# Optimization experiments

Measured on AMD Instinct MI355X. Metric: run time of the kernel, lower is better.

The kernel has to match this reference:

```python
import jax, jax.numpy as jnp
import numpy as np

T, B, L, S = 2048, 64, 32, 256
NEG = -1e30  # effective -inf, safe under logaddexp


def setup_inputs() -> dict:
    key = jax.random.key(0)
    k1, k2, k3 = jax.random.split(key, 3)
    inputs = jax.random.normal(k1, (T, B, L), dtype=jnp.float32)
    targets = jax.random.randint(k2, (B, S), 0, L)
    input_lengths = jnp.full((B,), T, dtype=jnp.int32)
    target_lengths = jnp.full((B,), S, dtype=jnp.int32)
    # learned transition matrix (param of ASGLoss); small random for a non-trivial test
    transition = 0.1 * jax.random.normal(k3, (L, L), dtype=jnp.float32)
    return {"transition": transition, "inputs": inputs, "targets": targets,
            "input_lengths": input_lengths, "target_lengths": target_lengths}


def _fcc_scores(transition, inputs, input_lengths):
    # Fully-connected forward: alpha_t[i] = emit_t[i] + logsumexp_j(alpha_{t-1}[j] + trans[i,j])
    alpha0 = inputs[0]  # [B, L]

    def step(alpha, emit):
        new = emit + jax.nn.logsumexp(alpha[:, None, :] + transition[None, :, :], axis=2)
        return new, new

    _, rest = jax.lax.scan(step, alpha0, inputs[1:])
    alphas = jnp.concatenate([alpha0[None], rest], axis=0)  # [T, B, L]
    b = jnp.arange(inputs.shape[1])
    # causal DP: alpha at t = len-1 is exactly the score for that length
    return jax.nn.logsumexp(alphas[input_lengths - 1, b], axis=-1)  # [B]


def _fac_scores(transition, inputs, targets, input_lengths, target_lengths):
    # Force-aligned forward over target positions s:
    # alpha_t[s] = emit_t[tgt_s] + logaddexp(alpha_{t-1}[s] + trans[tgt_s,tgt_s],
    #                                        alpha_{t-1}[s-1] + trans[tgt_s,tgt_{s-1}])
    Tn, Bn, _ = inputs.shape
    Sn = targets.shape[1]
    # gathered emissions for target labels: [T, B, S]
    emit = jnp.take_along_axis(inputs, jnp.broadcast_to(targets[None], (Tn, Bn, Sn)), axis=2)
    self_tr = transition[targets, targets]                       # [B, S] stay score
    prev = jnp.concatenate([targets[:, :1], targets[:, :-1]], 1)
    move_tr = transition[targets, prev]                          # [B, S] move score (s=0 unused)

    alpha0 = jnp.where((jnp.arange(Sn) == 0)[None, :], emit[0], NEG)  # only s=0 at t=0

    def step(alpha, e):
        stay = alpha + self_tr
        moved = jnp.concatenate(
            [jnp.full_like(alpha[:, :1], NEG), alpha[:, :-1] + move_tr[:, 1:]], axis=1)
        new = e + jnp.logaddexp(stay, moved)
        return new, new

    _, rest = jax.lax.scan(step, alpha0, emit[1:])
    alphas = jnp.concatenate([alpha0[None], rest], axis=0)  # [T, B, S]
    b = jnp.arange(Bn)
    return alphas[input_lengths - 1, b, target_lengths - 1]  # [B]


def reference(transition, inputs, targets, input_lengths, target_lengths):
    # original clamps targets to input length; S <= T here so it's a no-op
    fcc = _fcc_scores(transition, inputs, input_lengths)
    fac = _fac_scores(transition, inputs, targets, input_lengths, target_lengths)
    result = fcc - fac  # [B]
    return result.mean()  # reduction='mean'
```

## Files before the change

### kernel.cpp

```cpp
#include <hip/hip_runtime.h>
#include <math.h>

static constexpr int TB = 64;
static constexpr int LL = 32;
static constexpr int SS = 256;
static constexpr int STRIDE_T = TB * LL;

static constexpr int OF_FWD  = 0;
static constexpr int OF_BWD  = 33;
static constexpr int OF_FACF = 2178;
static constexpr int OF_FACB = 2498;
static constexpr int WSB     = 2818;

#define LN2F 0.69314718055994530942f
#define NEGF (-1e30f)

#define BARX() { asm volatile("s_waitcnt lgkmcnt(0)" ::: "memory"); \
                 __builtin_amdgcn_s_barrier(); \
                 asm volatile("" ::: "memory"); }

template<int CTL>
__device__ __forceinline__ float dpp_f(float x, float oldv) {
  return __int_as_float(__builtin_amdgcn_update_dpp(
      __float_as_int(oldv), __float_as_int(x), CTL, 0xF, 0xF, false));
}
template<int M>
__device__ __forceinline__ int rot_i(int x) {
  return __builtin_amdgcn_update_dpp(0, x, 0x120 + M, 0xF, 0xF, false);
}

typedef unsigned uint2v __attribute__((ext_vector_type(2)));
__device__ __forceinline__ float xsum16(float x) {
  uint2v r = __builtin_amdgcn_permlane16_swap(__float_as_uint(x), __float_as_uint(x), false, false);
  return __uint_as_float(r.x) + __uint_as_float(r.y);
}
__device__ __forceinline__ float xsum32(float x) {
  uint2v r = __builtin_amdgcn_permlane32_swap(__float_as_uint(x), __float_as_uint(x), false, false);
  return __uint_as_float(r.x) + __uint_as_float(r.y);
}
__device__ __forceinline__ float bperm(int addr, float src) {
  return __int_as_float(__builtin_amdgcn_ds_bpermute(addr, __float_as_int(src)));
}

template<int M>
struct Calib {
  __device__ static __forceinline__ void run(const float* trans, int lam, int i, float* Ec) {
    Ec[M] = __expf(trans[i * LL + rot_i<M>(lam)]);
    Calib<M + 1>::run(trans, lam, i, Ec);
  }
};
template<> struct Calib<16> {
  __device__ static __forceinline__ void run(const float*, int, int, float*) {}
};
template<int M>
struct CalibT {
  __device__ static __forceinline__ void run(const float* trans, int lam, int i, float* Ec) {
    Ec[M] = __expf(trans[rot_i<M>(lam) * LL + i]);
    CalibT<M + 1>::run(trans, lam, i, Ec);
  }
};
template<> struct CalibT<16> {
  __device__ static __forceinline__ void run(const float*, int, int, float*) {}
};

#define ROT_MUL(DST, SRC, COEF, ROT) \
  asm("v_mul_f32_dpp %0, %1, %2 row_ror:" #ROT " row_mask:0xf bank_mask:0xf" \
      : "=v"(DST) : "v"(SRC), "v"(COEF))
#define ROT_FMAC(ACC, SRC, COEF, ROT) \
  asm("v_fmac_f32_dpp %0, %1, %2 row_ror:" #ROT " row_mask:0xf bank_mask:0xf" \
      : "+v"(ACC) : "v"(SRC), "v"(COEF))

#define STEP16(EC) { \
  float a0 = EC[0] * A, a1, a2, a3, a4, a5, a6, a7; \
  ROT_MUL(a1, A, EC[1], 1); ROT_MUL(a2, A, EC[2], 2); ROT_MUL(a3, A, EC[3], 3); \
  ROT_MUL(a4, A, EC[4], 4); ROT_MUL(a5, A, EC[5], 5); ROT_MUL(a6, A, EC[6], 6); \
  ROT_MUL(a7, A, EC[7], 7); \
  ROT_FMAC(a0, A, EC[8], 8);   ROT_FMAC(a1, A, EC[9], 9); \
  ROT_FMAC(a2, A, EC[10], 10); ROT_FMAC(a3, A, EC[11], 11); \
  ROT_FMAC(a4, A, EC[12], 12); ROT_FMAC(a5, A, EC[13], 13); \
  ROT_FMAC(a6, A, EC[14], 14); ROT_FMAC(a7, A, EC[15], 15); \
  part = ((a0 + a1) + (a2 + a3)) + ((a4 + a5) + (a6 + a7)); }


#define FCC_RENORM() { \
  unsigned uu = (unsigned)__builtin_amdgcn_readfirstlane((int)__float_as_uint(A)); \
  int ex = (int)((uu >> 23) & 255) - 127; \
  A = ldexpf(A, -ex); Kt += ex; }

#define FCC_STEP_E(Q) { float part; STEP16(Ec1); A = eb[Q] * xsum16(part); }
#define FCC_STEP_O(Q) { float part; STEP16(Ec2); A = eb[Q] * xsum32(part); }

#define FCC_CONSUME16(PB) { \
  float eb[16]; \
  _Pragma("unroll") for (int q = 0; q < 16; ++q) eb[q] = sE[PB][q][(q & 1) ? lam1 : lam2]; \
  FCC_STEP_E(0); FCC_STEP_O(1); FCC_STEP_E(2); FCC_STEP_O(3); \
  FCC_STEP_E(4); FCC_STEP_O(5); FCC_STEP_E(6); FCC_STEP_O(7); \
  FCC_RENORM(); \
  FCC_STEP_E(8); FCC_STEP_O(9); FCC_STEP_E(10); FCC_STEP_O(11); \
  FCC_STEP_E(12); FCC_STEP_O(13); FCC_STEP_E(14); FCC_STEP_O(15); \
  FCC_RENORM(); }

#define FCC_TAIL16(PB, CNT) { \
  float eb[16]; \
  _Pragma("unroll") for (int q = 0; q < 16; ++q) eb[q] = sE[PB][q][(q & 1) ? lam1 : lam2]; \
  _Pragma("unroll") for (int q = 0; q < 16; ++q) { \
    if (q >= (CNT)) break; \
    if ((q & 1) == 0) { float part; STEP16(Ec1); A = eb[q] * xsum16(part); } \
    else              { float part; STEP16(Ec2); A = eb[q] * xsum32(part); } \
    if (q == 7) { FCC_RENORM(); } } }

#define FCC_BSTEP_A(Q) { A *= eb[Q]; float part; STEP16(E1T); A = xsum16(part); }
#define FCC_BSTEP_B(Q) { A *= eb[Q]; float part; STEP16(E2T); A = xsum32(part); }

#define FCC_BWDCON16(PB) { \
  float eb[16]; \
  _Pragma("unroll") for (int q = 0; q < 16; ++q) eb[q] = sE[PB][q][(q & 1) ? lam1 : lam2]; \
  FCC_BSTEP_A(15); FCC_BSTEP_B(14); FCC_BSTEP_A(13); FCC_BSTEP_B(12); \
  FCC_BSTEP_A(11); FCC_BSTEP_B(10); FCC_BSTEP_A(9);  FCC_BSTEP_B(8); \
  FCC_RENORM(); \
  FCC_BSTEP_A(7);  FCC_BSTEP_B(6);  FCC_BSTEP_A(5);  FCC_BSTEP_B(4); \
  FCC_BSTEP_A(3);  FCC_BSTEP_B(2);  FCC_BSTEP_A(1);  FCC_BSTEP_B(0); \
  FCC_RENORM(); }


#define FAC_STEP(E0, E1, E2, E3) { \
  float ap = dpp_f<0x138>(A3, 0.f);  \
  float n0 = (E0) * fmaf(MV0b,  ap, ST[0] * A0); \
  float n1 = (E1) * fmaf(MVl[1], A0, ST[1] * A1); \
  float n2 = (E2) * fmaf(MVl[2], A1, ST[2] * A2); \
  float n3 = (E3) * fmaf(MVl[3], A2, ST[3] * A3); \
  A0 = n0; A1 = n1; A2 = n2; A3 = n3; }

#define FAC_BOUNDARY() { \
  float maxA = fmaxf(fmaxf(A0, A1), fmaxf(A2, A3)); \
  if (maxA > 0.f) { \
    int ex = (int)((__float_as_uint(maxA) >> 23) & 255) - 127; \
    A0 = ldexpf(A0, -ex); A1 = ldexpf(A1, -ex); \
    A2 = ldexpf(A2, -ex); A3 = ldexpf(A3, -ex); \
    m += (float)ex; \
  } \
  float mp = dpp_f<0x138>(m, NEGF); m = (m == NEGF) ? mp : m; \
  mp = dpp_f<0x138>(m, NEGF);       m = (m == NEGF) ? mp : m; \
  mp = dpp_f<0x138>(m, NEGF); \
  float dlt = fminf(mp - m, 50.0f); \
  float Sin = exp2f(dlt); \
  MV0b = MVl[0] * Sin; }

#define FACF_CON16(PB) { \
  float4 Er[16]; \
  _Pragma("unroll") for (int r = 0; r < 16; ++r) Er[r] = sF[PB][r][l]; \
  _Pragma("unroll") for (int r = 0; r < 8; ++r) \
    FAC_STEP(Er[r].x, Er[r].y, Er[r].z, Er[r].w); \
  FAC_BOUNDARY(); \
  _Pragma("unroll") for (int r = 8; r < 16; ++r) \
    FAC_STEP(Er[r].x, Er[r].y, Er[r].z, Er[r].w); \
  FAC_BOUNDARY(); }

#define FACF_TAIL16(PB, CNT) { \
  float4 Er[16]; \
  _Pragma("unroll") for (int r = 0; r < 16; ++r) Er[r] = sF[PB][r][l]; \
  _Pragma("unroll") for (int r = 0; r < 16; ++r) { \
    if (r >= (CNT)) break; \
    FAC_STEP(Er[r].x, Er[r].y, Er[r].z, Er[r].w); \
    if (r == 7) { FAC_BOUNDARY(); } } }

#define FACB_BOUNDARY() { \
  float maxA = fmaxf(fmaxf(A0, A1), fmaxf(A2, A3)); \
  if (maxA > 0.f) { \
    int ex = (int)((__float_as_uint(maxA) >> 23) & 255) - 127; \
    A0 = ldexpf(A0, -ex); A1 = ldexpf(A1, -ex); \
    A2 = ldexpf(A2, -ex); A3 = ldexpf(A3, -ex); \
    m += (float)ex; \
  } \
  float mp = dpp_f<0x130>(m, NEGF); m = (m == NEGF) ? mp : m; \
  mp = dpp_f<0x130>(m, NEGF);       m = (m == NEGF) ? mp : m; \
  mp = dpp_f<0x130>(m, NEGF); \
  float dlt = fminf(mp - m, 50.0f); \
  MVn3b = MVn[3] * exp2f(dlt); }

#define FACB_STEP(Q) { \
    float en3 = dpp_f<0x130>(Er[Q].x, 0.f);  \
    float an  = dpp_f<0x130>(A0, 0.f); \
    float n0 = fmaf(Er[Q].y * MVn[0], A1, Er[Q].x * ST[0] * A0); \
    float n1 = fmaf(Er[Q].z * MVn[1], A2, Er[Q].y * ST[1] * A1); \
    float n2 = fmaf(Er[Q].w * MVn[2], A3, Er[Q].z * ST[2] * A2); \
    float n3 = fmaf(en3 * MVn3b,      an, Er[Q].w * ST[3] * A3); \
    A0 = n0; A1 = n1; A2 = n2; A3 = n3; }

#define FACB_CON16(PB) { \
  float4 Er[16]; \
  _Pragma("unroll") for (int r = 0; r < 16; ++r) Er[r] = sF[PB][r][l]; \
  FACB_STEP(15); FACB_STEP(14); FACB_STEP(13); FACB_STEP(12); \
  FACB_STEP(11); FACB_STEP(10); FACB_STEP(9);  FACB_STEP(8); \
  FACB_BOUNDARY(); \
  FACB_STEP(7);  FACB_STEP(6);  FACB_STEP(5);  FACB_STEP(4); \
  FACB_STEP(3);  FACB_STEP(2);  FACB_STEP(1);  FACB_STEP(0); \
  FACB_BOUNDARY(); }


#define HLD(Q, K) ({ \
  int tt_ = (isfwd ? (1 + 16 * (Q)) : (lenm1 - 16 * (Q) - 15)) + 2 * (K) + rowoff; \
  tt_ = tt_ < 0 ? 0 : (tt_ > lenm1 ? lenm1 : tt_); \
  gpl[(size_t)tt_ * STRIDE_T]; })

#define PROD_FCC(PB, KK, RV) { sE[PB][2 * (KK) + rowoff][lam1] = __expf(RV); }

#define PROD_FAC(PB, KK, RV) { \
  float e_ = __expf(RV); \
  float4 E0_, E1_; \
  E0_.x = bperm(adA[0], e_); E0_.y = bperm(adA[1], e_); \
  E0_.z = bperm(adA[2], e_); E0_.w = bperm(adA[3], e_); \
  E1_.x = bperm(adB[0], e_); E1_.y = bperm(adB[1], e_); \
  E1_.z = bperm(adB[2], e_); E1_.w = bperm(adB[3], e_); \
  sF[PB][2 * (KK)][l]     = E0_; \
  sF[PB][2 * (KK) + 1][l] = E1_; }

#define PRODUCE(PB, VA, VB) { \
  if (fac) { PROD_FAC(PB, kh, VA); PROD_FAC(PB, kh + 1, VB); } \
  else     { PROD_FCC(PB, kh, VA); PROD_FCC(PB, kh + 1, VB); } }


extern "C" __global__ __launch_bounds__(320, 1)
void asg_main(const float* __restrict__ trans, const float* __restrict__ inputs,
              const int* __restrict__ targets, const int* __restrict__ ilen,
              const int* __restrict__ tlen, float* __restrict__ ws) {
  const int tid = (int)threadIdx.x;
  const int w = tid >> 6;
  const int l = tid & 63;
  const int lam1 = l & 31;
  const int lam2 = (l & 15) | ((l >> 5) << 4);
  const int rowoff = l >> 5;

  const int role = (int)blockIdx.x >> 6;
  const int b    = (int)blockIdx.x & 63;

  const int len = ilen[b];
  const int lenm1 = len - 1;
  const int Lsteps = lenm1;
  const int nb = (Lsteps / 2) & ~15;
  const int nf = Lsteps - nb;
  const bool isfwd = (role == 0) || (role == 2);
  const int nsteps = isfwd ? nf : nb;
  const int nph = (nsteps + 15) >> 4;

  const float* gpl = inputs + (size_t)b * LL + lam1;
  float* P = ws + (size_t)b * WSB;

  __shared__ float  sE[2][16][32];
  __shared__ float4 sF[2][16][64];

  if (w == 0) {
    __builtin_amdgcn_s_setprio(1);

    if (role == 0) {
      float Ec1[16], Ec2[16];
      Ec1[0] = __expf(trans[lam2 * LL + lam1]);
      Ec2[0] = __expf(trans[lam1 * LL + lam2]);
      Calib<1>::run(trans, lam1, lam2, Ec1);
      Calib<1>::run(trans, lam2, lam1, Ec2);
      float A = __expf(inputs[(size_t)b * LL + lam1]);
      int Kt = 0;
      for (int p = 0; p < nph; p += 2) {
        BARX();
        { const int rem = nsteps - 16 * p;
          if (rem >= 16) { FCC_CONSUME16(0); } else { FCC_TAIL16(0, rem); } }
        BARX();
        if (p + 1 < nph) {
          const int rem = nsteps - 16 * (p + 1);
          if (rem >= 16) { FCC_CONSUME16(1); } else { FCC_TAIL16(1, rem); }
        }
      }
      const int par = nsteps & 1;
      const int idx = par ? lam2 : lam1;
      const bool wr = par ? ((l & 16) == 0) : (l < 32);
      if (wr) P[OF_FWD + idx] = A;
      if (l == 0) P[OF_FWD + 32] = (float)Kt;

    } else if (role == 1) {
      float E1T[16], E2T[16];
      E1T[0] = __expf(trans[lam1 * LL + lam2]);
      E2T[0] = __expf(trans[lam2 * LL + lam1]);
      CalibT<1>::run(trans, lam1, lam2, E1T);
      CalibT<1>::run(trans, lam2, lam1, E2T);
      float A = 1.f;
      int Kt = 0;
      for (int p = 0; p < nph; p += 2) {
        BARX();
        FCC_BWDCON16(0);
        BARX();
        if (p + 1 < nph) { FCC_BWDCON16(1); }
      }
      if (l < 32) P[OF_BWD + lam1] = A;
      if (l == 0) P[OF_BWD + 32] = (float)Kt;

    } else if (role == 2) {
      int tg[4];
      #pragma unroll
      for (int q = 0; q < 4; ++q) tg[q] = targets[b * SS + 4 * l + q];
      float ST[4], MVl[4];
      #pragma unroll
      for (int q = 0; q < 4; ++q) ST[q] = __expf(trans[tg[q] * LL + tg[q]]);
      MVl[0] = (l == 0) ? 0.f : __expf(trans[tg[0] * LL + targets[b * SS + 4 * l - 1]]);
      #pragma unroll
      for (int q = 1; q < 4; ++q) MVl[q] = __expf(trans[tg[q] * LL + tg[q - 1]]);

      float A0 = (l == 0) ? __expf(inputs[(size_t)b * LL + tg[0]]) : 0.f;
      float A1 = 0.f, A2 = 0.f, A3 = 0.f;
      float m  = (l == 0) ? 0.f : NEGF;
      float MV0b;
      FAC_BOUNDARY();

      for (int p = 0; p < nph; p += 2) {
        BARX();
        { const int rem = nsteps - 16 * p;
          if (rem >= 16) { FACF_CON16(0); } else { FACF_TAIL16(0, rem); } }
        BARX();
        if (p + 1 < nph) {
          const int rem = nsteps - 16 * (p + 1);
          if (rem >= 16) { FACF_CON16(1); } else { FACF_TAIL16(1, rem); }
        }
      }
      P[OF_FACF + 4 * l + 0] = A0;
      P[OF_FACF + 4 * l + 1] = A1;
      P[OF_FACF + 4 * l + 2] = A2;
      P[OF_FACF + 4 * l + 3] = A3;
      P[OF_FACF + 256 + l]   = m;

    } else {
      const int tl = tlen[b];
      const int fs = tl - 1;
      int tg[4];
      #pragma unroll
      for (int q = 0; q < 4; ++q) tg[q] = targets[b * SS + 4 * l + q];
      float ST[4], MVn[4];
      #pragma unroll
      for (int q = 0; q < 4; ++q) ST[q] = __expf(trans[tg[q] * LL + tg[q]]);
      MVn[0] = __expf(trans[tg[1] * LL + tg[0]]);
      MVn[1] = __expf(trans[tg[2] * LL + tg[1]]);
      MVn[2] = __expf(trans[tg[3] * LL + tg[2]]);
      int tgn3 = (l < 63) ? targets[b * SS + 4 * l + 4] : 0;
      MVn[3] = (l < 63) ? __expf(trans[tgn3 * LL + tg[3]]) : 0.f;

      float A0 = (4 * l + 0 == fs) ? 1.f : 0.f;
      float A1 = (4 * l + 1 == fs) ? 1.f : 0.f;
      float A2 = (4 * l + 2 == fs) ? 1.f : 0.f;
      float A3 = (4 * l + 3 == fs) ? 1.f : 0.f;
      float m  = (l == (fs >> 2)) ? 0.f : NEGF;
      float MVn3b;
      FACB_BOUNDARY();

      for (int p = 0; p < nph; p += 2) {
        BARX();
        FACB_CON16(0);
        BARX();
        if (p + 1 < nph) { FACB_CON16(1); }
      }
      P[OF_FACB + 4 * l + 0] = A0;
      P[OF_FACB + 4 * l + 1] = A1;
      P[OF_FACB + 4 * l + 2] = A2;
      P[OF_FACB + 4 * l + 3] = A3;
      P[OF_FACB + 256 + l]   = m;
    }

  } else {
    const int kh = 2 * (w - 1);
    const bool fac = (role >= 2);
    int adA[4] = {0, 0, 0, 0}, adB[4] = {0, 0, 0, 0};
    if (fac) {
      #pragma unroll
      for (int j = 0; j < 4; ++j) {
        int tg = targets[b * SS + 4 * l + j];
        adA[j] = tg * 4; adB[j] = adA[j] + 128;
      }
    }
    float R1a = HLD(0, kh), R1b = HLD(0, kh + 1);
    float R2a = HLD(1, kh), R2b = HLD(1, kh + 1);
    float R3a = HLD(2, kh), R3b = HLD(2, kh + 1);
    PRODUCE(0, R1a, R1b);
    R1a = R2a; R1b = R2b; R2a = R3a; R2b = R3b;
    R3a = HLD(3, kh); R3b = HLD(3, kh + 1);

    for (int p = 0; p < nph; p += 2) {
      BARX();
      if (p + 1 < nph) {
        float Na = HLD(p + 4, kh), Nb = HLD(p + 4, kh + 1);
        PRODUCE(1, R1a, R1b);
        R1a = R2a; R1b = R2b; R2a = R3a; R2b = R3b; R3a = Na; R3b = Nb;
      }
      BARX();
      if (p + 2 < nph) {
        float Na = HLD(p + 5, kh), Nb = HLD(p + 5, kh + 1);
        PRODUCE(0, R1a, R1b);
        R1a = R2a; R1b = R2b; R2a = R3a; R2b = R3b; R3a = Na; R3b = Nb;
      }
    }
  }
}


extern "C" __global__ __launch_bounds__(1024)
void asg_combine(const float* __restrict__ ws, float* __restrict__ out) {
  __shared__ float sd[TB];
  const int tid = (int)threadIdx.x;
  const int w = tid >> 6, l = tid & 63;

  for (int k = 0; k < 4; ++k) {
    const int b = w * 4 + k;
    const float* P = ws + (size_t)b * WSB;

    float al = (l < 32) ? P[OF_FWD + l] : 0.f;
    float vv = (l < 32) ? P[OF_BWD + l] : 0.f;
    float s = al * vv;
    #pragma unroll
    for (int mm = 1; mm < 64; mm <<= 1) s += __shfl_xor(s, mm);
    float fcc = __logf(s) + (P[OF_FWD + 32] + P[OF_BWD + 32]) * LN2F;

    float pa = P[OF_FACF + 4 * l + 0] * P[OF_FACB + 4 * l + 0]
             + P[OF_FACF + 4 * l + 1] * P[OF_FACB + 4 * l + 1]
             + P[OF_FACF + 4 * l + 2] * P[OF_FACB + 4 * l + 2]
             + P[OF_FACF + 4 * l + 3] * P[OF_FACB + 4 * l + 3];
    float sc = P[OF_FACF + 256 + l] + P[OF_FACB + 256 + l];
    float Ms = sc;
    #pragma unroll
    for (int mm = 1; mm < 64; mm <<= 1) Ms = fmaxf(Ms, __shfl_xor(Ms, mm));
    float pp = pa * exp2f(sc - Ms);
    #pragma unroll
    for (int mm = 1; mm < 64; mm <<= 1) pp += __shfl_xor(pp, mm);
    float fac = __logf(pp) + Ms * LN2F;

    if (l == 0) sd[b] = fcc - fac;
  }
  __syncthreads();
  if (tid < TB) {
    float d = sd[tid];
    #pragma unroll
    for (int mm = 1; mm < 64; mm <<= 1) d += __shfl_xor(d, mm);
    if (tid == 0) out[0] = d * (1.0f / TB);
  }
}


extern "C" void kernel_launch(void* const* d_in, const int* in_sizes, int n_in,
                              void* d_out, int out_size, void* d_ws, size_t ws_size,
                              hipStream_t stream) {
  const float* trans   = (const float*)d_in[0];
  const float* inputs  = (const float*)d_in[1];
  const int*   targets = (const int*)d_in[2];
  const int*   ilen    = (const int*)d_in[3];
  const int*   tlen    = (const int*)d_in[4];
  float* out = (float*)d_out;
  float* ws  = (float*)d_ws;

  asg_main<<<dim3(4 * TB), dim3(320), 0, stream>>>(trans, inputs, targets, ilen, tlen, ws);
  asg_combine<<<dim3(1), dim3(1024), 0, stream>>>(ws, out);
}
```

Measured before the change: 81.91 us.

## Split FCC recurrence into three segments with a matrix-propagated middle chunk

The fully-connected forward recurrence is split into three time segments instead of two: forward, backward and a new middle segment. The middle segment is computed as a 32x32 transfer matrix by 256 extra blocks, each propagating 8 unit-vector columns. The combine kernel multiplies the forward alpha by this matrix before taking the dot with the backward vector. This shortens the serial critical path of the FCC chain at the cost of doubling the grid, widening blocks to 512 threads with idle waves that only hit barriers, and adding a matrix-vector product in the combine step.

Measured after the change: 146.1 us. 1.78x slower.

```diff
diff --git a/kernel.cpp b/kernel.cpp
--- a/kernel.cpp
+++ b/kernel.cpp
@@ -8,6 +8,7 @@
 
 static constexpr int OF_FWD  = 0;
 static constexpr int OF_BWD  = 33;
+static constexpr int OF_MC   = 66;
 static constexpr int OF_FACF = 2178;
 static constexpr int OF_FACB = 2498;
 static constexpr int WSB     = 2818;
@@ -198,10 +199,15 @@
   FACB_BOUNDARY(); }
 
 
-#define HLD(Q, K) ({ \
-  int tt_ = (isfwd ? (1 + 16 * (Q)) : (lenm1 - 16 * (Q) - 15)) + 2 * (K) + rowoff; \
+#define HLDF(Q, K, T0) ({ \
+  int tt_ = (T0) + 16 * (Q) + 2 * (K) + rowoff; \
+  tt_ = tt_ > lenm1 ? lenm1 : tt_; \
+  gpl[(size_t)tt_ * STRIDE_T]; })
+#define HLDB(Q, K) ({ \
+  int tt_ = lenm1 - 16 * (Q) - 15 + 2 * (K) + rowoff; \
   tt_ = tt_ < 0 ? 0 : (tt_ > lenm1 ? lenm1 : tt_); \
   gpl[(size_t)tt_ * STRIDE_T]; })
+#define HLD2(Q, K) ( isfwd ? HLDF(Q, K, 1) : HLDB(Q, K) )
 
 #define PROD_FCC(PB, KK, RV) { sE[PB][2 * (KK) + rowoff][lam1] = __expf(RV); }
 
@@ -220,7 +226,7 @@
   else     { PROD_FCC(PB, kh, VA); PROD_FCC(PB, kh + 1, VB); } }
 
 
-extern "C" __global__ __launch_bounds__(320, 1)
+extern "C" __global__ __launch_bounds__(512, 1)
 void asg_main(const float* __restrict__ trans, const float* __restrict__ inputs,
               const int* __restrict__ targets, const int* __restrict__ ilen,
               const int* __restrict__ tlen, float* __restrict__ ws) {
@@ -230,24 +236,73 @@
   const int lam1 = l & 31;
   const int lam2 = (l & 15) | ((l >> 5) << 4);
   const int rowoff = l >> 5;
-
-  const int role = (int)blockIdx.x >> 6;
-  const int b    = (int)blockIdx.x & 63;
+  const int bid = (int)blockIdx.x;
+
+  __shared__ float  sE[2][16][32];
+  __shared__ float4 sF[2][16][64];
+
+  if (bid < 4 * TB) {
+    const int xcd = bid & 7, r = bid >> 3;
+    const int b = xcd + 8 * (r >> 2);
+    const int cb = r & 3;
+    const int len = ilen[b];
+    const int lenm1 = len - 1;
+    const int Lsteps = lenm1;
+    const int third = (Lsteps / 3) & ~15;
+    const int nf0 = Lsteps - 2 * third;
+    const int nph = third >> 4;
+    const int t0 = nf0 + 1;
+
+    const float* gpl = inputs + (size_t)b * LL + lam1;
+    float* P = ws + (size_t)b * WSB;
+
+    float Ec1[16], Ec2[16];
+    Ec1[0] = __expf(trans[lam2 * LL + lam1]);
+    Ec2[0] = __expf(trans[lam1 * LL + lam2]);
+    Calib<1>::run(trans, lam1, lam2, Ec1);
+    Calib<1>::run(trans, lam2, lam1, Ec2);
+
+    const int col = 8 * cb + w;
+    float A = (lam1 == col) ? 1.f : 0.f;
+    int Kt = 0;
+
+    float R1 = HLDF(0, w, t0), R2 = HLDF(1, w, t0), R3 = HLDF(2, w, t0);
+    PROD_FCC(0, w, R1);
+    R1 = R2; R2 = R3; R3 = HLDF(3, w, t0);
+
+    for (int p = 0; p < nph; p += 2) {
+      BARX();
+      if (p + 1 < nph) { float N = HLDF(p + 4, w, t0); PROD_FCC(1, w, R1);
+                         R1 = R2; R2 = R3; R3 = N; }
+      FCC_CONSUME16(0);
+      BARX();
+      if (p + 2 < nph) { float N = HLDF(p + 5, w, t0); PROD_FCC(0, w, R1);
+                         R1 = R2; R2 = R3; R3 = N; }
+      if (p + 1 < nph) { FCC_CONSUME16(1); }
+    }
+    if (l < 32) P[OF_MC + col * 33 + lam1] = A;
+    if (l == 0) P[OF_MC + col * 33 + 32] = (float)Kt;
+    return;
+  }
+
+  const int rid  = bid - 4 * TB;
+  const int role = rid >> 6;
+  const int b    = rid & 63;
 
   const int len = ilen[b];
   const int lenm1 = len - 1;
   const int Lsteps = lenm1;
-  const int nb = (Lsteps / 2) & ~15;
-  const int nf = Lsteps - nb;
+  const int third = (Lsteps / 3) & ~15;
+  const int nf0 = Lsteps - 2 * third;
+  const int nbf = (Lsteps / 2) & ~15;
+  const int nff = Lsteps - nbf;
   const bool isfwd = (role == 0) || (role == 2);
-  const int nsteps = isfwd ? nf : nb;
+  const int nsteps = (role == 0) ? nf0 : (role == 1) ? third
+                    : (role == 2) ? nff : nbf;
   const int nph = (nsteps + 15) >> 4;
 
   const float* gpl = inputs + (size_t)b * LL + lam1;
   float* P = ws + (size_t)b * WSB;
-
-  __shared__ float  sE[2][16][32];
-  __shared__ float4 sF[2][16][64];
 
   if (w == 0) {
     __builtin_amdgcn_s_setprio(1);
@@ -362,7 +417,7 @@
       P[OF_FACB + 256 + l]   = m;
     }
 
-  } else {
+  } else if (w <= 4) {
     const int kh = 2 * (w - 1);
     const bool fac = (role >= 2);
     int adA[4] = {0, 0, 0, 0}, adB[4] = {0, 0, 0, 0};
@@ -373,27 +428,31 @@
         adA[j] = tg * 4; adB[j] = adA[j] + 128;
       }
     }
-    float R1a = HLD(0, kh), R1b = HLD(0, kh + 1);
-    float R2a = HLD(1, kh), R2b = HLD(1, kh + 1);
-    float R3a = HLD(2, kh), R3b = HLD(2, kh + 1);
+    float R1a = HLD2(0, kh), R1b = HLD2(0, kh + 1);
+    float R2a = HLD2(1, kh), R2b = HLD2(1, kh + 1);
+    float R3a = HLD2(2, kh), R3b = HLD2(2, kh + 1);
     PRODUCE(0, R1a, R1b);
     R1a = R2a; R1b = R2b; R2a = R3a; R2b = R3b;
-    R3a = HLD(3, kh); R3b = HLD(3, kh + 1);
+    R3a = HLD2(3, kh); R3b = HLD2(3, kh + 1);
 
     for (int p = 0; p < nph; p += 2) {
       BARX();
       if (p + 1 < nph) {
-        float Na = HLD(p + 4, kh), Nb = HLD(p + 4, kh + 1);
+        float Na = HLD2(p + 4, kh), Nb = HLD2(p + 4, kh + 1);
         PRODUCE(1, R1a, R1b);
         R1a = R2a; R1b = R2b; R2a = R3a; R2b = R3b; R3a = Na; R3b = Nb;
       }
       BARX();
       if (p + 2 < nph) {
-        float Na = HLD(p + 5, kh), Nb = HLD(p + 5, kh + 1);
+        float Na = HLD2(p + 5, kh), Nb = HLD2(p + 5, kh + 1);
         PRODUCE(0, R1a, R1b);
         R1a = R2a; R1b = R2b; R2a = R3a; R2b = R3b; R3a = Na; R3b = Nb;
       }
     }
+
+  } else {
+    const int I = (nph + 1) >> 1;
+    for (int i = 0; i < I; ++i) { BARX(); BARX(); }
   }
 }
 
@@ -408,12 +467,23 @@
     const int b = w * 4 + k;
     const float* P = ws + (size_t)b * WSB;
 
-    float al = (l < 32) ? P[OF_FWD + l] : 0.f;
+    float al  = (l < 32) ? P[OF_FWD + l] : 0.f;
+    float Kacc = P[OF_FWD + 32] + P[OF_BWD + 32];
+
+    float KA = (l < 32) ? P[OF_MC + 33 * l + 32] : -3.0e38f;
+    float Km = KA;
+    #pragma unroll
+    for (int s = 1; s < 64; s <<= 1) Km = fmaxf(Km, __shfl_xor(Km, s));
+    float wj = (l < 32) ? al * exp2f(KA - Km) : 0.f;
+    float t1 = 0.f;
+    for (int j = 0; j < 32; ++j) t1 += P[OF_MC + 33 * j + (l & 31)] * __shfl(wj, j);
+    Kacc += Km;
+
     float vv = (l < 32) ? P[OF_BWD + l] : 0.f;
-    float s = al * vv;
+    float s = vv * t1;
     #pragma unroll
     for (int mm = 1; mm < 64; mm <<= 1) s += __shfl_xor(s, mm);
-    float fcc = __logf(s) + (P[OF_FWD + 32] + P[OF_BWD + 32]) * LN2F;
+    float fcc = __logf(s) + Kacc * LN2F;
 
     float pa = P[OF_FACF + 4 * l + 0] * P[OF_FACB + 4 * l + 0]
              + P[OF_FACF + 4 * l + 1] * P[OF_FACB + 4 * l + 1]
@@ -451,6 +521,6 @@
   float* out = (float*)d_out;
   float* ws  = (float*)d_ws;
 
-  asg_main<<<dim3(4 * TB), dim3(320), 0, stream>>>(trans, inputs, targets, ilen, tlen, ws);
+  asg_main<<<dim3(8 * TB), dim3(512), 0, stream>>>(trans, inputs, targets, ilen, tlen, ws);
   asg_combine<<<dim3(1), dim3(1024), 0, stream>>>(ws, out);
 }
```
